# Optimization experiments

Hardware: AMD Instinct MI355X
Metric: run time of the kernel (lower is better)

Reference implementation:

```python
import jax, jax.numpy as jnp
import numpy as np

B, T, E = 2, 2048, 1024
H, D = 16, 64
NH = H * D  # num_hiddens
EPS = 1e-5


def setup_inputs() -> dict:
    key = jax.random.key(0)
    ks = jax.random.split(key, 8)
    s = 1.0 / np.sqrt(E)
    inputs_q = jax.random.normal(ks[0], (B, T, E), dtype=jnp.float32)
    inputs_kv = jax.random.normal(ks[1], (B, T, E), dtype=jnp.float32)
    # torch Linear weights: [out_features, in_features]
    wq = jax.random.uniform(ks[2], (NH, E), jnp.float32, -s, s)
    wk = jax.random.uniform(ks[3], (NH, E), jnp.float32, -s, s)
    wv = jax.random.uniform(ks[4], (NH, E), jnp.float32, -s, s)
    wo = jax.random.uniform(ks[5], (E, NH), jnp.float32, -1.0 / np.sqrt(NH), 1.0 / np.sqrt(NH))
    q_ln_scale = jnp.ones((NH,), jnp.float32)
    q_ln_bias = jnp.zeros((NH,), jnp.float32)
    k_ln_scale = jnp.ones((NH,), jnp.float32)
    k_ln_bias = jnp.zeros((NH,), jnp.float32)
    # causal mask, broadcastable over heads: [B, 1, T, T]
    mask = jnp.broadcast_to(jnp.tril(jnp.ones((T, T), dtype=bool)), (B, 1, T, T))
    return dict(inputs_q=inputs_q, inputs_kv=inputs_kv, mask=mask,
                wq=wq, wk=wk, wv=wv, wo=wo,
                q_ln_scale=q_ln_scale, q_ln_bias=q_ln_bias,
                k_ln_scale=k_ln_scale, k_ln_bias=k_ln_bias)


def _layernorm(x, scale, bias):
    mu = jnp.mean(x, axis=-1, keepdims=True)
    var = jnp.var(x, axis=-1, keepdims=True)
    return (x - mu) * jax.lax.rsqrt(var + EPS) * scale + bias


def reference(inputs_q, inputs_kv, mask, wq, wk, wv, wo,
              q_ln_scale, q_ln_bias, k_ln_scale, k_ln_bias):
    q = jnp.einsum('bte,he->bth', inputs_q, wq)   # [B,T,NH]
    k = jnp.einsum('bte,he->bth', inputs_kv, wk)
    q = _layernorm(q, q_ln_scale, q_ln_bias)
    k = _layernorm(k, k_ln_scale, k_ln_bias)
    v = jnp.einsum('bte,he->bth', inputs_kv, wv)
    q = q.reshape(B, T, H, D)
    k = k.reshape(B, T, H, D)
    v = v.reshape(B, T, H, D)
    attn = jnp.einsum('bthd,bThd->bhtT', q, k) * (1.0 / np.sqrt(D))
    attn = jnp.where(mask, attn, -jnp.inf)
    p = jax.nn.softmax(attn, axis=-1)
    out = jnp.einsum('bhtT,bThd->bthd', p, v).reshape(B, T, NH)
    return jnp.einsum('bth,eh->bte', out, wo)
```

## Files before the change

### kernel.cpp

```cpp
#include <hip/hip_runtime.h>
#include <stdint.h>

#define BB 2
#define TT 2048
#define EE 1024
#define HH 16
#define DD 64
#define NHH 1024
#define BT 4096
#define NT 32

typedef unsigned short u16_t;
typedef __bf16 bf16_t;
typedef bf16_t bf16x8 __attribute__((ext_vector_type(8)));
typedef bf16_t bf16x4 __attribute__((ext_vector_type(4)));
typedef float f32x4 __attribute__((ext_vector_type(4)));

__device__ __forceinline__ u16_t f2bf(float f) {
  union { float f; uint32_t u; } v; v.f = f;
  return (u16_t)((v.u + 0x7fffu + ((v.u >> 16) & 1u)) >> 16);
}

__device__ __forceinline__ uint32_t cvtpk_bf16(float lo, float hi) {
  uint32_t r;
  asm("v_cvt_pk_bf16_f32 %0, %1, %2" : "=v"(r) : "v"(lo), "v"(hi));
  return r;
}

__device__ __forceinline__ void gl_lds16(const u16_t* g, u16_t* l) {
  __builtin_amdgcn_global_load_lds(
      (const __attribute__((address_space(1))) uint32_t*)g,
      (__attribute__((address_space(3))) uint32_t*)l, 16, 0, 0);
}

__global__ __launch_bounds__(256) void cvt_all(const float* __restrict__ inq,
                                               const float* __restrict__ inkv,
                                               const float* __restrict__ wq,
                                               const float* __restrict__ wk,
                                               const float* __restrict__ wv,
                                               const float* __restrict__ wo,
                                               u16_t* __restrict__ Xq,
                                               u16_t* __restrict__ Xkv,
                                               u16_t* __restrict__ Wqkv,
                                               u16_t* __restrict__ Wo) {
  const int NX = BT * NHH / 4;
  const int NW = NHH * EE / 4;
  const int total = 2 * NX + 4 * NW;
  for (int idx = blockIdx.x * 256 + threadIdx.x; idx < total; idx += gridDim.x * 256) {
    const float* src; u16_t* dst; int off;
    if (idx < NX)            { src = inq;  dst = Xq;  off = idx; }
    else if (idx < 2 * NX)   { src = inkv; dst = Xkv; off = idx - NX; }
    else if (idx < 2 * NX + NW)     { src = wq; dst = Wqkv;                       off = idx - 2 * NX; }
    else if (idx < 2 * NX + 2 * NW) { src = wk; dst = Wqkv + (size_t)NHH * EE;    off = idx - (2 * NX + NW); }
    else if (idx < 2 * NX + 3 * NW) { src = wv; dst = Wqkv + (size_t)2 * NHH * EE; off = idx - (2 * NX + 2 * NW); }
    else                            { src = wo; dst = Wo;                          off = idx - (2 * NX + 3 * NW); }
    float4 v = ((const float4*)src)[off];
    ushort4 o;
    o.x = f2bf(v.x); o.y = f2bf(v.y); o.z = f2bf(v.z); o.w = f2bf(v.w);
    ((ushort4*)dst)[off] = o;
  }
}

__global__ __launch_bounds__(256, 3) void gemm_qkv(const u16_t* __restrict__ Xq,
                                                   const u16_t* __restrict__ Xkv,
                                                   const u16_t* __restrict__ Wqkv,
                                                   u16_t* __restrict__ Qpre,
                                                   u16_t* __restrict__ Kpre,
                                                   u16_t* __restrict__ Vb) {
  __shared__ __align__(16) u16_t As[128 * 64];
  __shared__ __align__(16) u16_t Bs[128 * 64];
  const int tid = threadIdx.x;
  const int lane = tid & 63;
  const int w = tid >> 6;
  const int wm = w >> 1, wn = w & 1;
  const int nt = blockIdx.x, mt = blockIdx.y;
  const int l15 = lane & 15, l4 = lane >> 4;
  const int band = nt >> 3;
  const u16_t* A = (band == 0) ? Xq : Xkv;
  u16_t* C = (band == 0) ? Qpre : (band == 1) ? Kpre : Vb;
  const int ncol0 = (nt & 7) * 128;

  f32x4 acc[4][4] = {};
  for (int ks = 0; ks < 16; ++ks) {
    const int k0 = ks << 6;
#pragma unroll
    for (int i = 0; i < 4; ++i) {
      int ci = i * 256 + w * 64 + lane;
      int row = ci >> 3, c8 = ci & 7;
      int c8s = c8 ^ (row & 7);
      gl_lds16(A + (size_t)(mt * 128 + row) * EE + k0 + c8s * 8,
               &As[(i * 256 + w * 64) * 8]);
      gl_lds16(Wqkv + (size_t)(nt * 128 + row) * EE + k0 + c8s * 8,
               &Bs[(i * 256 + w * 64) * 8]);
    }
    __syncthreads();
#pragma unroll
    for (int kt = 0; kt < 2; ++kt) {
      bf16x8 af[4], bfr[4];
#pragma unroll
      for (int m = 0; m < 4; ++m) {
        int r = wm * 64 + m * 16 + l15;
        af[m] = *(const bf16x8*)&As[r * 64 + ((kt * 4 + l4) ^ (r & 7)) * 8];
      }
#pragma unroll
      for (int n = 0; n < 4; ++n) {
        int r = wn * 64 + n * 16 + l15;
        bfr[n] = *(const bf16x8*)&Bs[r * 64 + ((kt * 4 + l4) ^ (r & 7)) * 8];
      }
#pragma unroll
      for (int m = 0; m < 4; ++m)
#pragma unroll
        for (int n = 0; n < 4; ++n)
          acc[m][n] = __builtin_amdgcn_mfma_f32_16x16x32_bf16(af[m], bfr[n], acc[m][n], 0, 0, 0);
    }
    __syncthreads();
  }
#pragma unroll
  for (int m = 0; m < 4; ++m)
#pragma unroll
    for (int n = 0; n < 4; ++n)
#pragma unroll
      for (int r = 0; r < 4; ++r) {
        int row = mt * 128 + wm * 64 + m * 16 + l4 * 4 + r;
        int col = ncol0 + wn * 64 + n * 16 + l15;
        C[(size_t)row * NHH + col] = f2bf(acc[m][n][r]);
      }
}

__global__ __launch_bounds__(256, 3) void gemm_out(const u16_t* __restrict__ A,
                                                   const u16_t* __restrict__ W,
                                                   float* __restrict__ C) {
  __shared__ __align__(16) u16_t As[64 * 64];
  __shared__ __align__(16) u16_t Bs[128 * 64];
  const int tid = threadIdx.x;
  const int lane = tid & 63;
  const int w = tid >> 6;
  const int wm = w >> 1, wn = w & 1;
  const int nt = blockIdx.x, mt = blockIdx.y;
  const int l15 = lane & 15, l4 = lane >> 4;

  f32x4 acc[2][4] = {};
  for (int ks = 0; ks < 16; ++ks) {
    const int k0 = ks << 6;
#pragma unroll
    for (int i = 0; i < 6; ++i) {
      int ci = i * 256 + w * 64 + lane;
      if (i < 2) {
        int row = ci >> 3, c8s = (ci & 7) ^ ((ci >> 3) & 7);
        gl_lds16(A + (size_t)(mt * 64 + row) * NHH + k0 + c8s * 8,
                 &As[(i * 256 + w * 64) * 8]);
      } else {
        int cj = ci - 512;
        int row = cj >> 3, c8s = (cj & 7) ^ ((cj >> 3) & 7);
        gl_lds16(W + (size_t)(nt * 128 + row) * NHH + k0 + c8s * 8,
                 &Bs[(i * 256 + w * 64 - 512) * 8]);
      }
    }
    __syncthreads();
#pragma unroll
    for (int kt = 0; kt < 2; ++kt) {
      bf16x8 af[2], bfr[4];
#pragma unroll
      for (int m = 0; m < 2; ++m) {
        int r = wm * 32 + m * 16 + l15;
        af[m] = *(const bf16x8*)&As[r * 64 + ((kt * 4 + l4) ^ (r & 7)) * 8];
      }
#pragma unroll
      for (int n = 0; n < 4; ++n) {
        int r = wn * 64 + n * 16 + l15;
        bfr[n] = *(const bf16x8*)&Bs[r * 64 + ((kt * 4 + l4) ^ (r & 7)) * 8];
      }
#pragma unroll
      for (int m = 0; m < 2; ++m)
#pragma unroll
        for (int n = 0; n < 4; ++n)
          acc[m][n] = __builtin_amdgcn_mfma_f32_16x16x32_bf16(af[m], bfr[n], acc[m][n], 0, 0, 0);
    }
    __syncthreads();
  }
#pragma unroll
  for (int m = 0; m < 2; ++m)
#pragma unroll
    for (int n = 0; n < 4; ++n)
#pragma unroll
      for (int r = 0; r < 4; ++r) {
        int row = mt * 64 + wm * 32 + m * 16 + l4 * 4 + r;
        int col = nt * 128 + wn * 64 + n * 16 + l15;
        C[(size_t)row * NHH + col] = acc[m][n][r];
      }
}

__global__ __launch_bounds__(256) void ln_both(const u16_t* __restrict__ Qpre,
                                               const u16_t* __restrict__ Kpre,
                                               const float* __restrict__ qs,
                                               const float* __restrict__ qb,
                                               const float* __restrict__ ks,
                                               const float* __restrict__ kb,
                                               u16_t* __restrict__ Qln,
                                               u16_t* __restrict__ Kln) {
  int which = blockIdx.y;
  const u16_t* X = which ? Kpre : Qpre;
  const float* scale = which ? ks : qs;
  const float* bias = which ? kb : qb;
  u16_t* Y = which ? Kln : Qln;
  int row = blockIdx.x;
  int tid = threadIdx.x;
  ushort4 v4 = ((const ushort4*)(X + (size_t)row * NHH))[tid];
  float x[4];
  {
    union { uint32_t u; float f; } c;
    c.u = (uint32_t)v4.x << 16; x[0] = c.f;
    c.u = (uint32_t)v4.y << 16; x[1] = c.f;
    c.u = (uint32_t)v4.z << 16; x[2] = c.f;
    c.u = (uint32_t)v4.w << 16; x[3] = c.f;
  }
  float s = x[0] + x[1] + x[2] + x[3];
  float sq = x[0] * x[0] + x[1] * x[1] + x[2] * x[2] + x[3] * x[3];
#pragma unroll
  for (int m = 1; m < 64; m <<= 1) {
    s += __shfl_xor(s, m);
    sq += __shfl_xor(sq, m);
  }
  __shared__ float ss[4], ssq[4];
  int w = tid >> 6;
  if ((tid & 63) == 0) { ss[w] = s; ssq[w] = sq; }
  __syncthreads();
  s = ss[0] + ss[1] + ss[2] + ss[3];
  sq = ssq[0] + ssq[1] + ssq[2] + ssq[3];
  float mean = s * (1.0f / 1024.0f);
  float var = sq * (1.0f / 1024.0f) - mean * mean;
  float rstd = rsqrtf(var + 1e-5f);
  float4 sc = ((const float4*)scale)[tid];
  float4 bi = ((const float4*)bias)[tid];
  ushort4 o;
  o.x = f2bf((x[0] - mean) * rstd * sc.x + bi.x);
  o.y = f2bf((x[1] - mean) * rstd * sc.y + bi.y);
  o.z = f2bf((x[2] - mean) * rstd * sc.z + bi.z);
  o.w = f2bf((x[3] - mean) * rstd * sc.w + bi.w);
  ((ushort4*)Y)[(size_t)row * 256 + tid] = o;
}

__global__ __launch_bounds__(256) void transpose_v(const u16_t* __restrict__ V,
                                                   u16_t* __restrict__ Vt) {
  __shared__ u16_t tile[64][72];
  int tt = blockIdx.x, bh = blockIdx.y;
  int b = bh >> 4, h = bh & 15;
  int tid = threadIdx.x;
#pragma unroll
  for (int i = 0; i < 4; ++i) {
    int idx = i * 256 + tid;
    int t = idx >> 4, c4 = idx & 15;
    ushort4 v = *(const ushort4*)&V[(size_t)(b * TT + tt * 64 + t) * NHH + h * 64 + c4 * 4];
    *(ushort4*)&tile[t][c4 * 4] = v;
  }
  __syncthreads();
#pragma unroll
  for (int i = 0; i < 4; ++i) {
    int idx = i * 256 + tid;
    int d = idx >> 4, c4 = idx & 15;
    ushort4 o;
    o.x = tile[c4 * 4 + 0][d];
    o.y = tile[c4 * 4 + 1][d];
    o.z = tile[c4 * 4 + 2][d];
    o.w = tile[c4 * 4 + 3][d];
    *(ushort4*)&Vt[((size_t)bh * 64 + d) * TT + tt * 64 + c4 * 4] = o;
  }
}

__global__ __launch_bounds__(512, 4) void attn_fwd(const u16_t* __restrict__ Q,
                                                   const u16_t* __restrict__ K,
                                                   const u16_t* __restrict__ Vt,
                                                   u16_t* __restrict__ O) {
  __shared__ __align__(16) u16_t Ks[128 * 64];
  __shared__ __align__(16) u16_t Vs[64 * 128];
  const int bh = blockIdx.x, pr = blockIdx.y;
  const int b = bh >> 4, h = bh & 15;
  const int tid = threadIdx.x, lane = tid & 63, w = tid >> 6;
  const int l15 = lane & 15, l4 = lane >> 4;
  const float SCALE = 0.125f * 1.44269504f;

  const int qtH = NT - 1 - pr;
  const int my_qt = (w < 4) ? qtH : pr;
  const int q0 = my_qt * 64 + (w & 3) * 16;
  const int myq = q0 + l15;

  bf16x8 qf[2];
#pragma unroll
  for (int kt = 0; kt < 2; ++kt) {
    bf16x8 t = *(const bf16x8*)&Q[(size_t)(b * TT + myq) * NHH + h * 64 + kt * 32 + l4 * 8];
    union { bf16x8 v; uint32_t u[4]; } tt;
    tt.v = t;
#pragma unroll
    for (int d2 = 0; d2 < 4; ++d2) {
      union { uint32_t u; float f; } lo, hi;
      lo.u = tt.u[d2] << 16;
      hi.u = tt.u[d2] & 0xffff0000u;
      tt.u[d2] = cvtpk_bf16(lo.f * SCALE, hi.f * SCALE);
    }
    qf[kt] = tt.v;
  }

  f32x4 accO[4] = {};
  float mrow = -1e30f, lrow = 0.f;

  const int nkv = (qtH + 2) >> 1;
  for (int j = 0; j < nkv; ++j) {
    const int kb = j << 7;
#pragma unroll
    for (int i = 0; i < 2; ++i) {
      int ci = i * 512 + tid;
      int rowk = ci >> 3, c8s = (ci & 7) ^ (rowk & 7);
      gl_lds16(K + (size_t)(b * TT + kb + rowk) * NHH + h * 64 + c8s * 8, &Ks[ci * 8]);
      int rowv = ci >> 4, c16s = (ci & 15) ^ (rowv & 15);
      gl_lds16(Vt + ((size_t)bh * 64 + rowv) * TT + kb + c16s * 8, &Vs[ci * 8]);
    }
    __syncthreads();

    if (kb <= q0 + 15) {
      const int rel = q0 + 15 - kb;
      const int nact = min(8, (rel >> 4) + 1);
      const int ktlim = min(4, (rel >> 5) + 1);
      const bool domask = (kb + 127 > q0);

      f32x4 s[8];
#pragma unroll
      for (int n = 0; n < 8; ++n) {
        if (n < nact) {
          s[n] = (f32x4){0.f, 0.f, 0.f, 0.f};
#pragma unroll
          for (int kt = 0; kt < 2; ++kt) {
            int r = n * 16 + l15;
            bf16x8 kf = *(const bf16x8*)&Ks[r * 64 + ((kt * 4 + l4) ^ (r & 7)) * 8];
            s[n] = __builtin_amdgcn_mfma_f32_16x16x32_bf16(kf, qf[kt], s[n], 0, 0, 0);
          }
        }
      }
      if (domask) {
#pragma unroll
        for (int n = 0; n < 8; ++n)
          if (n < nact)
#pragma unroll
            for (int r = 0; r < 4; ++r)
              if (kb + n * 16 + l4 * 4 + r > myq) s[n][r] = -3e38f;
      }
      float tmax = -3e38f;
#pragma unroll
      for (int n = 0; n < 8; ++n)
        if (n < nact)
#pragma unroll
          for (int r = 0; r < 4; ++r) tmax = fmaxf(tmax, s[n][r]);
      tmax = fmaxf(tmax, __shfl_xor(tmax, 16));
      tmax = fmaxf(tmax, __shfl_xor(tmax, 32));
      if (__any(tmax > mrow + 8.f)) {
        float mnew = fmaxf(mrow, tmax);
        float scl = exp2f(mrow - mnew);
        lrow *= scl;
        mrow = mnew;
#pragma unroll
        for (int r = 0; r < 4; ++r) {
          float sr = __shfl(scl, l4 * 4 + r);
#pragma unroll
          for (int dn = 0; dn < 4; ++dn) accO[dn][r] *= sr;
        }
      }
      float tsum = 0.f;
#pragma unroll
      for (int n = 0; n < 8; ++n)
        if (n < nact)
#pragma unroll
          for (int r = 0; r < 4; ++r) {
            float p = exp2f(s[n][r] - mrow);
            s[n][r] = p;
            tsum += p;
          }
      tsum += __shfl_xor(tsum, 16);
      tsum += __shfl_xor(tsum, 32);
      lrow += tsum;
#pragma unroll
      for (int n = 0; n < 8; ++n)
        if (n >= nact && n < 2 * ktlim) s[n] = (f32x4){0.f, 0.f, 0.f, 0.f};

#pragma unroll
      for (int kt = 0; kt < 4; ++kt) {
        if (kt < ktlim) {
          union { uint32_t u[4]; bf16x8 v; } pa;
          pa.u[0] = cvtpk_bf16(s[2 * kt][0], s[2 * kt][1]);
          pa.u[1] = cvtpk_bf16(s[2 * kt][2], s[2 * kt][3]);
          pa.u[2] = cvtpk_bf16(s[2 * kt + 1][0], s[2 * kt + 1][1]);
          pa.u[3] = cvtpk_bf16(s[2 * kt + 1][2], s[2 * kt + 1][3]);
#pragma unroll
          for (int dn = 0; dn < 4; ++dn) {
            int drow = dn * 16 + l15;
            int c0 = (kt * 4 + (l4 >> 1)) ^ (drow & 15);
            int c1 = (kt * 4 + 2 + (l4 >> 1)) ^ (drow & 15);
            int sub = (l4 & 1) * 4;
            union { bf16x4 h[2]; bf16x8 v; } vf;
            vf.h[0] = *(const bf16x4*)&Vs[drow * 128 + c0 * 8 + sub];
            vf.h[1] = *(const bf16x4*)&Vs[drow * 128 + c1 * 8 + sub];
            accO[dn] = __builtin_amdgcn_mfma_f32_16x16x32_bf16(pa.v, vf.v, accO[dn], 0, 0, 0);
          }
        }
      }
    }
    __syncthreads();
  }
#pragma unroll
  for (int r = 0; r < 4; ++r) {
    float lr = __shfl(lrow, l4 * 4 + r);
    float rinv = 1.0f / lr;
    int row = b * TT + q0 + l4 * 4 + r;
#pragma unroll
    for (int dn = 0; dn < 4; ++dn)
      O[(size_t)row * NHH + h * 64 + dn * 16 + l15] = f2bf(accO[dn][r] * rinv);
  }
}

extern "C" void kernel_launch(void* const* d_in, const int* in_sizes, int n_in,
                              void* d_out, int out_size, void* d_ws, size_t ws_size,
                              hipStream_t stream) {
  const float* inq = (const float*)d_in[0];
  const float* inkv = (const float*)d_in[1];
  const float* wq = (const float*)d_in[3];
  const float* wk = (const float*)d_in[4];
  const float* wv = (const float*)d_in[5];
  const float* wo = (const float*)d_in[6];
  const float* qs = (const float*)d_in[7];
  const float* qb = (const float*)d_in[8];
  const float* kls = (const float*)d_in[9];
  const float* klb = (const float*)d_in[10];
  float* out = (float*)d_out;

  uint8_t* ws = (uint8_t*)d_ws;
  const size_t SZ_X = (size_t)BT * NHH * 2;
  const size_t SZ_W = (size_t)NHH * EE * 2;
  u16_t* Xq   = (u16_t*)(ws);
  u16_t* Xkv  = (u16_t*)(ws + SZ_X);
  u16_t* Wqkv = (u16_t*)(ws + 2 * SZ_X);
  u16_t* Wo   = (u16_t*)(ws + 2 * SZ_X + 3 * SZ_W);
  u16_t* Qpre = (u16_t*)(ws + 2 * SZ_X + 4 * SZ_W);
  u16_t* Kpre = (u16_t*)(ws + 3 * SZ_X + 4 * SZ_W);
  u16_t* Vb   = (u16_t*)(ws + 4 * SZ_X + 4 * SZ_W);
  u16_t* Qln  = (u16_t*)(ws + 5 * SZ_X + 4 * SZ_W);
  u16_t* Kln  = (u16_t*)(ws + 6 * SZ_X + 4 * SZ_W);
  u16_t* Vt   = (u16_t*)(ws + 7 * SZ_X + 4 * SZ_W);
  u16_t* AOut = (u16_t*)(ws + 8 * SZ_X + 4 * SZ_W);

  cvt_all<<<3072, 256, 0, stream>>>(inq, inkv, wq, wk, wv, wo, Xq, Xkv, Wqkv, Wo);

  gemm_qkv<<<dim3(24, 32), 256, 0, stream>>>(Xq, Xkv, Wqkv, Qpre, Kpre, Vb);

  ln_both<<<dim3(BT, 2), 256, 0, stream>>>(Qpre, Kpre, qs, qb, kls, klb, Qln, Kln);

  transpose_v<<<dim3(TT / 64, BB * HH), 256, 0, stream>>>(Vb, Vt);

  attn_fwd<<<dim3(BB * HH, NT / 2), 512, 0, stream>>>(Qln, Kln, Vt, AOut);

  gemm_out<<<dim3(8, 64), 256, 0, stream>>>(AOut, Wo, out);
}
```

Before: 237.1 us.

## Double-buffer K/V tiles in attention and prefetch next tile during compute

```diff
diff --git a/kernel.cpp b/kernel.cpp
--- a/kernel.cpp
+++ b/kernel.cpp
@@ -271,8 +271,8 @@
                                                    const u16_t* __restrict__ K,
                                                    const u16_t* __restrict__ Vt,
                                                    u16_t* __restrict__ O) {
-  __shared__ __align__(16) u16_t Ks[128 * 64];
-  __shared__ __align__(16) u16_t Vs[64 * 128];
+  __shared__ __align__(16) u16_t Ks[2][128 * 64];
+  __shared__ __align__(16) u16_t Vs[2][64 * 128];
   const int bh = blockIdx.x, pr = blockIdx.y;
   const int b = bh >> 4, h = bh & 15;
   const int tid = threadIdx.x, lane = tid & 63, w = tid >> 6;
@@ -304,17 +304,33 @@
   float mrow = -1e30f, lrow = 0.f;
 
   const int nkv = (qtH + 2) >> 1;
-  for (int j = 0; j < nkv; ++j) {
-    const int kb = j << 7;
+
+  auto stage_kv = [&](int j, int bi) {
+    const int kb_ = j << 7;
 #pragma unroll
     for (int i = 0; i < 2; ++i) {
       int ci = i * 512 + tid;
       int rowk = ci >> 3, c8s = (ci & 7) ^ (rowk & 7);
-      gl_lds16(K + (size_t)(b * TT + kb + rowk) * NHH + h * 64 + c8s * 8, &Ks[ci * 8]);
-      int rowv = ci >> 4, c16s = (ci & 15) ^ (rowv & 15);
-      gl_lds16(Vt + ((size_t)bh * 64 + rowv) * TT + kb + c16s * 8, &Vs[ci * 8]);
-    }
-    __syncthreads();
+      gl_lds16(K + (size_t)(b * TT + kb_ + rowk) * NHH + h * 64 + c8s * 8,
+               &Ks[bi][ci * 8]);
+      int rowv = ci >> 4, c16s = (ci & 15) ^ ((rowv >> 1) & 7);
+      gl_lds16(Vt + ((size_t)bh * 64 + rowv) * TT + kb_ + c16s * 8,
+               &Vs[bi][ci * 8]);
+    }
+  };
+
+  stage_kv(0, 0);
+  for (int j = 0; j < nkv; ++j) {
+    const int kb = j << 7;
+    const int bi = j & 1;
+    if (j + 1 < nkv) {
+      stage_kv(j + 1, bi ^ 1);
+      asm volatile("s_waitcnt vmcnt(4)" ::: "memory");
+    } else {
+      asm volatile("s_waitcnt vmcnt(0)" ::: "memory");
+    }
+    __builtin_amdgcn_s_barrier();
+    __builtin_amdgcn_sched_barrier(0);
 
     if (kb <= q0 + 15) {
       const int rel = q0 + 15 - kb;
@@ -323,6 +339,7 @@
       const bool domask = (kb + 127 > q0);
 
       f32x4 s[8];
+      __builtin_amdgcn_s_setprio(1);
 #pragma unroll
       for (int n = 0; n < 8; ++n) {
         if (n < nact) {
@@ -330,11 +347,12 @@
 #pragma unroll
           for (int kt = 0; kt < 2; ++kt) {
             int r = n * 16 + l15;
-            bf16x8 kf = *(const bf16x8*)&Ks[r * 64 + ((kt * 4 + l4) ^ (r & 7)) * 8];
+            bf16x8 kf = *(const bf16x8*)&Ks[bi][r * 64 + ((kt * 4 + l4) ^ (r & 7)) * 8];
             s[n] = __builtin_amdgcn_mfma_f32_16x16x32_bf16(kf, qf[kt], s[n], 0, 0, 0);
           }
         }
       }
+      __builtin_amdgcn_s_setprio(0);
       if (domask) {
 #pragma unroll
         for (int n = 0; n < 8; ++n)
@@ -380,6 +398,7 @@
       for (int n = 0; n < 8; ++n)
         if (n >= nact && n < 2 * ktlim) s[n] = (f32x4){0.f, 0.f, 0.f, 0.f};
 
+      __builtin_amdgcn_s_setprio(1);
 #pragma unroll
       for (int kt = 0; kt < 4; ++kt) {
         if (kt < ktlim) {
@@ -391,18 +410,20 @@
 #pragma unroll
           for (int dn = 0; dn < 4; ++dn) {
             int drow = dn * 16 + l15;
-            int c0 = (kt * 4 + (l4 >> 1)) ^ (drow & 15);
-            int c1 = (kt * 4 + 2 + (l4 >> 1)) ^ (drow & 15);
-            int sub = (l4 & 1) * 4;
+            int vm = ((drow >> 1) & 7) << 1;
+            int pg0 = (kt * 8 + l4) ^ vm;
+            int pg1 = (kt * 8 + 4 + l4) ^ vm;
             union { bf16x4 h[2]; bf16x8 v; } vf;
-            vf.h[0] = *(const bf16x4*)&Vs[drow * 128 + c0 * 8 + sub];
-            vf.h[1] = *(const bf16x4*)&Vs[drow * 128 + c1 * 8 + sub];
+            vf.h[0] = *(const bf16x4*)&Vs[bi][drow * 128 + pg0 * 4];
+            vf.h[1] = *(const bf16x4*)&Vs[bi][drow * 128 + pg1 * 4];
             accO[dn] = __builtin_amdgcn_mfma_f32_16x16x32_bf16(pa.v, vf.v, accO[dn], 0, 0, 0);
           }
         }
       }
-    }
-    __syncthreads();
+      __builtin_amdgcn_s_setprio(0);
+    }
+    __builtin_amdgcn_sched_barrier(0);
+    __builtin_amdgcn_s_barrier();
   }
 #pragma unroll
   for (int r = 0; r < 4; ++r) {
```

Result: no change. 236.1 us (-0.4%).

## Split KV range across wave halves per query tile with LDS merge

Applied to the files above, without the earlier changes.

```diff
diff --git a/kernel.cpp b/kernel.cpp
--- a/kernel.cpp
+++ b/kernel.cpp
@@ -267,21 +267,21 @@
   }
 }
 
-__global__ __launch_bounds__(512, 4) void attn_fwd(const u16_t* __restrict__ Q,
+__global__ __launch_bounds__(512, 6) void attn_fwd(const u16_t* __restrict__ Q,
                                                    const u16_t* __restrict__ K,
                                                    const u16_t* __restrict__ Vt,
                                                    u16_t* __restrict__ O) {
-  __shared__ __align__(16) u16_t Ks[128 * 64];
-  __shared__ __align__(16) u16_t Vs[64 * 128];
-  const int bh = blockIdx.x, pr = blockIdx.y;
+  __shared__ __align__(16) u16_t Ks[2][64 * 64];
+  __shared__ __align__(16) u16_t Vs[2][64 * 64];
+  const int bh = blockIdx.x;
+  const int qt = NT - 1 - (int)blockIdx.y;
   const int b = bh >> 4, h = bh & 15;
   const int tid = threadIdx.x, lane = tid & 63, w = tid >> 6;
   const int l15 = lane & 15, l4 = lane >> 4;
+  const int qsub = w & 3, par = w >> 2;
   const float SCALE = 0.125f * 1.44269504f;
 
-  const int qtH = NT - 1 - pr;
-  const int my_qt = (w < 4) ? qtH : pr;
-  const int q0 = my_qt * 64 + (w & 3) * 16;
+  const int q0 = qt * 64 + qsub * 16;
   const int myq = q0 + l15;
 
   bf16x8 qf[2];
@@ -300,44 +300,62 @@
     qf[kt] = tt.v;
   }
 
+  const int ci = tid;
+  const int rowk = ci >> 3;
+  const int c8k = (ci & 7) ^ (rowk & 7);
+  const int c8v = (ci & 7) ^ ((rowk >> 1) & 7);
+  const u16_t* kp = K + (size_t)(b * TT + rowk) * NHH + h * 64 + c8k * 8;
+  const u16_t* vp = Vt + ((size_t)bh * 64 + rowk) * TT + c8v * 8;
+  u16_t* kdst0 = &Ks[0][ci * 8];
+  u16_t* kdst1 = &Ks[1][ci * 8];
+  u16_t* vdst0 = &Vs[0][ci * 8];
+  u16_t* vdst1 = &Vs[1][ci * 8];
+  const u16_t* myK = Ks[par];
+  const u16_t* myV = Vs[par];
+
   f32x4 accO[4] = {};
   float mrow = -1e30f, lrow = 0.f;
 
-  const int nkv = (qtH + 2) >> 1;
-  for (int j = 0; j < nkv; ++j) {
-    const int kb = j << 7;
-#pragma unroll
-    for (int i = 0; i < 2; ++i) {
-      int ci = i * 512 + tid;
-      int rowk = ci >> 3, c8s = (ci & 7) ^ (rowk & 7);
-      gl_lds16(K + (size_t)(b * TT + kb + rowk) * NHH + h * 64 + c8s * 8, &Ks[ci * 8]);
-      int rowv = ci >> 4, c16s = (ci & 15) ^ (rowv & 15);
-      gl_lds16(Vt + ((size_t)bh * 64 + rowv) * TT + kb + c16s * 8, &Vs[ci * 8]);
-    }
+  const int ntile = qt + 1;
+  const int nph = (ntile + 1) >> 1;
+
+  for (int ph = 0; ph < nph; ++ph) {
+    const int t1ok = (2 * ph + 1) < ntile;
+    gl_lds16(kp, kdst0);
+    gl_lds16(vp, vdst0);
+    if (t1ok) {
+      gl_lds16(kp + 64 * NHH, kdst1);
+      gl_lds16(vp + 64, vdst1);
+    }
+    kp += 128 * NHH;
+    vp += 128;
     __syncthreads();
 
-    if (kb <= q0 + 15) {
-      const int rel = q0 + 15 - kb;
-      const int nact = min(8, (rel >> 4) + 1);
-      const int ktlim = min(4, (rel >> 5) + 1);
-      const bool domask = (kb + 127 > q0);
-
-      f32x4 s[8];
-#pragma unroll
-      for (int n = 0; n < 8; ++n) {
+    const int t = 2 * ph + par;
+    if (t < ntile) {
+      const int kb = t * 64;
+      const bool masked = (t == qt);
+      const int nact = masked ? (qsub + 1) : 4;
+      const int ktlim = masked ? ((qsub >> 1) + 1) : 2;
+
+      f32x4 s[4];
+      __builtin_amdgcn_s_setprio(1);
+#pragma unroll
+      for (int n = 0; n < 4; ++n) {
         if (n < nact) {
           s[n] = (f32x4){0.f, 0.f, 0.f, 0.f};
 #pragma unroll
           for (int kt = 0; kt < 2; ++kt) {
             int r = n * 16 + l15;
-            bf16x8 kf = *(const bf16x8*)&Ks[r * 64 + ((kt * 4 + l4) ^ (r & 7)) * 8];
+            bf16x8 kf = *(const bf16x8*)&myK[r * 64 + ((kt * 4 + l4) ^ (r & 7)) * 8];
             s[n] = __builtin_amdgcn_mfma_f32_16x16x32_bf16(kf, qf[kt], s[n], 0, 0, 0);
           }
         }
       }
-      if (domask) {
-#pragma unroll
-        for (int n = 0; n < 8; ++n)
+      __builtin_amdgcn_s_setprio(0);
+      if (masked) {
+#pragma unroll
+        for (int n = 0; n < 4; ++n)
           if (n < nact)
 #pragma unroll
             for (int r = 0; r < 4; ++r)
@@ -345,7 +363,7 @@
       }
       float tmax = -3e38f;
 #pragma unroll
-      for (int n = 0; n < 8; ++n)
+      for (int n = 0; n < 4; ++n)
         if (n < nact)
 #pragma unroll
           for (int r = 0; r < 4; ++r) tmax = fmaxf(tmax, s[n][r]);
@@ -365,7 +383,7 @@
       }
       float tsum = 0.f;
 #pragma unroll
-      for (int n = 0; n < 8; ++n)
+      for (int n = 0; n < 4; ++n)
         if (n < nact)
 #pragma unroll
           for (int r = 0; r < 4; ++r) {
@@ -377,11 +395,12 @@
       tsum += __shfl_xor(tsum, 32);
       lrow += tsum;
 #pragma unroll
-      for (int n = 0; n < 8; ++n)
+      for (int n = 0; n < 4; ++n)
         if (n >= nact && n < 2 * ktlim) s[n] = (f32x4){0.f, 0.f, 0.f, 0.f};
 
-#pragma unroll
-      for (int kt = 0; kt < 4; ++kt) {
+      __builtin_amdgcn_s_setprio(1);
+#pragma unroll
+      for (int kt = 0; kt < 2; ++kt) {
         if (kt < ktlim) {
           union { uint32_t u[4]; bf16x8 v; } pa;
           pa.u[0] = cvtpk_bf16(s[2 * kt][0], s[2 * kt][1]);
@@ -391,27 +410,59 @@
 #pragma unroll
           for (int dn = 0; dn < 4; ++dn) {
             int drow = dn * 16 + l15;
-            int c0 = (kt * 4 + (l4 >> 1)) ^ (drow & 15);
-            int c1 = (kt * 4 + 2 + (l4 >> 1)) ^ (drow & 15);
-            int sub = (l4 & 1) * 4;
-            union { bf16x4 h[2]; bf16x8 v; } vf;
-            vf.h[0] = *(const bf16x4*)&Vs[drow * 128 + c0 * 8 + sub];
-            vf.h[1] = *(const bf16x4*)&Vs[drow * 128 + c1 * 8 + sub];
+            int vm = l15 & 14;
+            int pg0 = (kt * 8 + l4) ^ vm;
+            int pg1 = (kt * 8 + 4 + l4) ^ vm;
+            union { bf16x4 hh[2]; bf16x8 v; } vf;
+            vf.hh[0] = *(const bf16x4*)&myV[drow * 64 + pg0 * 4];
+            vf.hh[1] = *(const bf16x4*)&myV[drow * 64 + pg1 * 4];
             accO[dn] = __builtin_amdgcn_mfma_f32_16x16x32_bf16(pa.v, vf.v, accO[dn], 0, 0, 0);
           }
         }
       }
+      __builtin_amdgcn_s_setprio(0);
     }
     __syncthreads();
   }
-#pragma unroll
-  for (int r = 0; r < 4; ++r) {
-    float lr = __shfl(lrow, l4 * 4 + r);
-    float rinv = 1.0f / lr;
-    int row = b * TT + q0 + l4 * 4 + r;
-#pragma unroll
-    for (int dn = 0; dn < 4; ++dn)
-      O[(size_t)row * NHH + h * 64 + dn * 16 + l15] = f2bf(accO[dn][r] * rinv);
+
+  float* xch = (float*)&Ks[0][0];
+  if (par == 1) {
+    float* dst = xch + (qsub * 64 + lane) * 20;
+#pragma unroll
+    for (int dn = 0; dn < 4; ++dn) *(f32x4*)(dst + dn * 4) = accO[dn];
+    if (l4 == 0) {
+      xch[5120 + qsub * 32 + l15 * 2] = mrow;
+      xch[5120 + qsub * 32 + l15 * 2 + 1] = lrow;
+    }
+  } else {
+    if (l4 == 0) {
+      xch[5248 + qsub * 32 + l15 * 2] = mrow;
+      xch[5248 + qsub * 32 + l15 * 2 + 1] = lrow;
+    }
+  }
+  __syncthreads();
+  if (par == 0) {
+    const float* src = xch + (qsub * 64 + lane) * 20;
+    f32x4 acc1[4];
+#pragma unroll
+    for (int dn = 0; dn < 4; ++dn) acc1[dn] = *(const f32x4*)(src + dn * 4);
+#pragma unroll
+    for (int r = 0; r < 4; ++r) {
+      int q = l4 * 4 + r;
+      float m0 = xch[5248 + qsub * 32 + q * 2];
+      float l0 = xch[5248 + qsub * 32 + q * 2 + 1];
+      float m1 = xch[5120 + qsub * 32 + q * 2];
+      float l1 = xch[5120 + qsub * 32 + q * 2 + 1];
+      float mM = fmaxf(m0, m1);
+      float s0 = exp2f(m0 - mM), s1 = exp2f(m1 - mM);
+      float rinv = 1.0f / (l0 * s0 + l1 * s1);
+      int row = b * TT + q0 + q;
+#pragma unroll
+      for (int dn = 0; dn < 4; ++dn) {
+        float o = (accO[dn][r] * s0 + acc1[dn][r] * s1) * rinv;
+        O[(size_t)row * NHH + h * 64 + dn * 16 + l15] = f2bf(o);
+      }
+    }
   }
 }
 
@@ -453,7 +504,7 @@
 
   transpose_v<<<dim3(TT / 64, BB * HH), 256, 0, stream>>>(Vb, Vt);
 
-  attn_fwd<<<dim3(BB * HH, NT / 2), 512, 0, stream>>>(Qln, Kln, Vt, AOut);
+  attn_fwd<<<dim3(BB * HH, NT), 512, 0, stream>>>(Qln, Kln, Vt, AOut);
 
   gemm_out<<<dim3(8, 64), 256, 0, stream>>>(AOut, Wo, out);
 }
```

Measured after the change: 229.9 us. 3.0% less time.
